# Performance work log

Measured on AMD Instinct MI355X. Metric: run time of the kernel, lower is better.

The kernel has to match this reference:

```python
import jax, jax.numpy as jnp
import numpy as np

B, T, DIM = 2, 2048, 1024
H, KVH, HD = 16, 4, 64
RANK = 32
QMAX = 31.0            # int6 signed: (1 << 5) - 1
SIGMA = 12.85          # MATRIX_QUANT_CLIP_SIGMAS
ROPE_BASE = 10000.0
LORA_SCALE = 1.0


def fake_quant_int6_rowwise(w):
    """Per-row int6 RTN fake-quant with clip-candidate search + STE, as in
    _quantize_rowwise_rtn / fake_quantize_int8_per_row (bits=6, no hessian)."""
    t = w.astype(jnp.float32)
    row_std = jnp.maximum(jnp.std(t, axis=1), 1e-8)                 # unbiased=False
    row_absmax = jnp.maximum(jnp.max(jnp.abs(t), axis=1), 1.0 / QMAX)
    # candidates: clip1 = max(std*sigma, absmax/qmax); clip2 = absmax (== initial best)
    s1 = jnp.maximum(jnp.maximum(row_std * SIGMA, row_absmax / QMAX) / QMAX, 1.0 / QMAX)
    s2 = jnp.maximum(row_absmax / QMAX, 1.0 / QMAX)
    q1 = jnp.clip(jnp.round(t / s1[:, None]), -QMAX, QMAX)
    q2 = jnp.clip(jnp.round(t / s2[:, None]), -QMAX, QMAX)
    e1 = jnp.mean((q1 * s1[:, None] - t) ** 2, axis=1)
    e2 = jnp.mean((q2 * s2[:, None] - t) ** 2, axis=1)
    use1 = e1 < e2  # torch keeps earlier/initial candidate on ties
    q = jnp.where(use1[:, None], q1, q2)
    s = jnp.where(use1, s1, s2)
    s = s.astype(jnp.float16).astype(jnp.float32)  # INT8_PER_ROW_SCALE_DTYPE
    w_deq = q * s[:, None]
    return w + jax.lax.stop_gradient(w_deq - w)   # straight-through estimator


def rope_tables(seq_len, head_dim):
    inv_freq = 1.0 / ROPE_BASE ** (np.arange(0, head_dim, 2, dtype=np.float32) / head_dim)
    freqs = np.arange(seq_len, dtype=np.float32)[:, None] * inv_freq[None, :]  # [T, HD/2]
    return jnp.asarray(np.cos(freqs)), jnp.asarray(np.sin(freqs))


def apply_rope(x, cos, sin):
    # x: [B, h, T, HD]; cos/sin: [T, HD/2]; rope_dims=0 -> rotate full head dim
    half = x.shape[-1] // 2
    x1, x2 = x[..., :half], x[..., half:]
    c = cos[None, None, :, :]
    s = sin[None, None, :, :]
    return jnp.concatenate([x1 * c + x2 * s, -x1 * s + x2 * c], axis=-1)


def setup_inputs() -> dict:
    key = jax.random.key(0)
    ks = jax.random.split(key, 16)
    d = {
        'x': jax.random.normal(ks[0], (B, T, DIM), jnp.float32),
        'Wq': jax.random.normal(ks[1], (DIM, DIM), jnp.float32) * 0.02,
        'Wk': jax.random.normal(ks[2], (KVH * HD, DIM), jnp.float32) * 0.02,
        'Wv': jax.random.normal(ks[3], (KVH * HD, DIM), jnp.float32) * 0.02,
        'Wo': jax.random.normal(ks[4], (DIM, DIM), jnp.float32) * 0.02,
        'qA': jax.random.normal(ks[5], (DIM, RANK), jnp.float32) * 0.02,
        'qB': jax.random.normal(ks[6], (RANK, DIM), jnp.float32) * 0.01,
        'kA': jax.random.normal(ks[7], (DIM, RANK), jnp.float32) * 0.02,
        'kB': jax.random.normal(ks[8], (RANK, KVH * HD), jnp.float32) * 0.01,
        'vA': jax.random.normal(ks[9], (DIM, RANK), jnp.float32) * 0.02,
        'vB': jax.random.normal(ks[10], (RANK, KVH * HD), jnp.float32) * 0.01,
        'pA': jax.random.normal(ks[11], (DIM, RANK), jnp.float32) * 0.02,
        'pB': jax.random.normal(ks[12], (RANK, DIM), jnp.float32) * 0.01,
        'q_gain': jnp.ones((H,), jnp.float32),
        'head_gate': jnp.ones((H,), jnp.float32),
    }
    return d


def reference(x, Wq, Wk, Wv, Wo, qA, qB, kA, kB, vA, vB, pA, pB, q_gain, head_gate):
    b, t, d = x.shape
    # QKV projections: fake-quantized base weight + LoRA low-rank add
    q = x @ fake_quant_int6_rowwise(Wq).T + LORA_SCALE * ((x @ qA) @ qB)
    k = x @ fake_quant_int6_rowwise(Wk).T + LORA_SCALE * ((x @ kA) @ kB)
    v = x @ fake_quant_int6_rowwise(Wv).T + LORA_SCALE * ((x @ vA) @ vB)

    q = q.reshape(b, t, H, HD).transpose(0, 2, 1, 3)      # [B, H, T, HD]
    k = k.reshape(b, t, KVH, HD).transpose(0, 2, 1, 3)    # [B, KVH, T, HD]
    v = v.reshape(b, t, KVH, HD).transpose(0, 2, 1, 3)

    cos, sin = rope_tables(t, HD)
    q = apply_rope(q, cos, sin) * q_gain[None, :, None, None]
    k = apply_rope(k, cos, sin)

    # GQA: expand kv heads to match query heads
    rep = H // KVH
    k = jnp.repeat(k, rep, axis=1)
    v = jnp.repeat(v, rep, axis=1)

    scores = jnp.einsum('bhqd,bhkd->bhqk', q, k) / np.sqrt(HD).astype(np.float32)
    causal = jnp.tril(jnp.ones((t, t), bool))
    scores = jnp.where(causal[None, None], scores, jnp.float32(-1e30))
    attn = jax.nn.softmax(scores, axis=-1)
    y = jnp.einsum('bhqk,bhkd->bhqd', attn, v)             # [B, H, T, HD]
    y = y * head_gate[None, :, None, None]
    y = y.transpose(0, 2, 1, 3).reshape(b, t, d)

    out = y @ fake_quant_int6_rowwise(Wo).T + LORA_SCALE * ((y @ pA) @ pB)
    return out
```

## Files before the change

### kernel.cpp

```cpp
#include <hip/hip_runtime.h>
#include <hip/hip_fp16.h>

#define Bc   2
#define Tc   2048
#define DIMc 1024
#define Hc   16
#define KVHc 4
#define HDc  64
#define Mc   4096

typedef unsigned short u16;
typedef __attribute__((ext_vector_type(8))) short short8;
typedef __attribute__((ext_vector_type(8))) __bf16 bf16x8;
typedef __attribute__((ext_vector_type(2))) __bf16 bf16x2;
typedef __attribute__((ext_vector_type(4))) float f32x4;
typedef __attribute__((ext_vector_type(4))) unsigned short u16x4;

typedef const __attribute__((address_space(1))) void* gas_t;
typedef __attribute__((address_space(3))) void* las_t;

#define L2E 1.4426950408889634f
#define L2B 0.41524101186092035f

__device__ inline float bf2f(u16 u) {
    unsigned int x = ((unsigned int)u) << 16;
    return __builtin_bit_cast(float, x);
}
__device__ inline u16 f2bf(float f) {
    unsigned int x = __builtin_bit_cast(unsigned int, f);
    x += 0x7fffu + ((x >> 16) & 1u);
    return (u16)(x >> 16);
}
__device__ inline unsigned int pkbf(float a, float b) {
#if __has_builtin(__builtin_amdgcn_cvt_pk_bf16_f32)
    bf16x2 r = __builtin_amdgcn_cvt_pk_bf16_f32(a, b);
    return __builtin_bit_cast(unsigned int, r);
#else
    return (unsigned int)f2bf(a) | ((unsigned int)f2bf(b) << 16);
#endif
}
__device__ inline u16x4 pk4(float a, float b, float c, float d) {
    uint2 u; u.x = pkbf(a, b); u.y = pkbf(c, d);
    return __builtin_bit_cast(u16x4, u);
}
__device__ inline float fexp2(float x) {
#if __has_builtin(__builtin_amdgcn_exp2f)
    return __builtin_amdgcn_exp2f(x);
#else
    return exp2f(x);
#endif
}
__device__ inline bf16x8 ld8(const u16* p) {
    return __builtin_bit_cast(bf16x8, *(const short8*)p);
}
__device__ inline f32x4 mfma16(bf16x8 a, bf16x8 b, f32x4 c) {
    return __builtin_amdgcn_mfma_f32_16x16x32_bf16(a, b, c, 0, 0, 0);
}
__device__ inline void gl_lds16(const u16* g, u16* l) {
    __builtin_amdgcn_global_load_lds((gas_t)g, (las_t)l, 16, 0, 0);
}

__global__ __launch_bounds__(256) void prep_kernel(
    const float* __restrict__ x,
    const float* __restrict__ qA, const float* __restrict__ kA,
    const float* __restrict__ vA, const float* __restrict__ pA,
    const float* __restrict__ qB, const float* __restrict__ kB,
    const float* __restrict__ vB, const float* __restrict__ pB,
    u16* __restrict__ x_bf, float* __restrict__ L)
{
    __shared__ __align__(16) u16 Ns[64 * 40];
    __shared__ __align__(16) u16 Ks[64 * 40];
    const int bx = blockIdx.x;
    const int tid = threadIdx.x;

    if (bx < 4096) {
        const int i = bx * 256 + tid;
        float4 v = ((const float4*)x)[i];
        ((u16x4*)x_bf)[i] = pk4(v.x, v.y, v.z, v.w);
        return;
    }
    const int lb = bx - 4096;
    const int mt = lb >> 4, kt = lb & 15;
    const int m0 = mt * 64, k0 = kt * 64;
    const float* Apt; const float* Bpt; int bdim, nnb;
    if (m0 < 1024)      { Apt = qA; Bpt = qB; bdim = 1024; nnb = m0; }
    else if (m0 < 1280) { Apt = kA; Bpt = kB; bdim = 256;  nnb = m0 - 1024; }
    else if (m0 < 1536) { Apt = vA; Bpt = vB; bdim = 256;  nnb = m0 - 1280; }
    else                { Apt = pA; Bpt = pB; bdim = 1024; nnb = m0 - 1536; }

    {
        const int row = tid >> 2, c0 = (tid & 3) * 8;
        const float4 f0 = *(const float4*)(Apt + (size_t)(k0 + row) * 32 + c0);
        const float4 f1 = *(const float4*)(Apt + (size_t)(k0 + row) * 32 + c0 + 4);
        *(u16x4*)&Ks[row * 40 + c0]     = pk4(f0.x, f0.y, f0.z, f0.w);
        *(u16x4*)&Ks[row * 40 + c0 + 4] = pk4(f1.x, f1.y, f1.z, f1.w);
    }
    {
        const int col = tid & 63;
        const int r0 = (tid >> 6) * 8;
        #pragma unroll
        for (int i = 0; i < 8; i++)
            Ns[col * 40 + r0 + i] = f2bf(Bpt[(size_t)(r0 + i) * bdim + nnb + col]);
    }
    __syncthreads();
    const int wave = tid >> 6, lane = tid & 63;
    const int quad = lane >> 4, l16 = lane & 15;
    const int wm = wave >> 1, wn = wave & 1;
    bf16x8 a0 = ld8(&Ns[(wm * 32 + l16) * 40 + quad * 8]);
    bf16x8 a1 = ld8(&Ns[(wm * 32 + 16 + l16) * 40 + quad * 8]);
    bf16x8 b0 = ld8(&Ks[(wn * 32 + l16) * 40 + quad * 8]);
    bf16x8 b1 = ld8(&Ks[(wn * 32 + 16 + l16) * 40 + quad * 8]);
    f32x4 c00 = {}, c01 = {}, c10 = {}, c11 = {};
    c00 = mfma16(a0, b0, c00);
    c01 = mfma16(a0, b1, c01);
    c10 = mfma16(a1, b0, c10);
    c11 = mfma16(a1, b1, c11);
    #pragma unroll
    for (int r = 0; r < 4; r++) {
        const size_t row_a = (size_t)(m0 + wm * 32 + quad * 4 + r) * 1024;
        const size_t row_b = (size_t)(m0 + wm * 32 + 16 + quad * 4 + r) * 1024;
        L[row_a + k0 + wn * 32 + l16]      = c00[r];
        L[row_a + k0 + wn * 32 + 16 + l16] = c01[r];
        L[row_b + k0 + wn * 32 + l16]      = c10[r];
        L[row_b + k0 + wn * 32 + 16 + l16] = c11[r];
    }
}

__device__ inline float block_sum(float v, volatile float* red) {
    #pragma unroll
    for (int off = 32; off; off >>= 1) v += __shfl_xor(v, off);
    __syncthreads();
    if ((threadIdx.x & 63) == 0) red[threadIdx.x >> 6] = v;
    __syncthreads();
    return red[0] + red[1] + red[2] + red[3];
}
__device__ inline float block_max(float v, volatile float* red) {
    #pragma unroll
    for (int off = 32; off; off >>= 1) v = fmaxf(v, __shfl_xor(v, off));
    __syncthreads();
    if ((threadIdx.x & 63) == 0) red[threadIdx.x >> 6] = v;
    __syncthreads();
    return fmaxf(fmaxf(red[0], red[1]), fmaxf(red[2], red[3]));
}

__global__ __launch_bounds__(256) void quant_kernel(
    const float* __restrict__ Wq, const float* __restrict__ Wk,
    const float* __restrict__ Wv, const float* __restrict__ Wo,
    const float* __restrict__ L,
    u16* __restrict__ Wqkv_b, u16* __restrict__ Wo_b)
{
    __shared__ float red[4];
    const int rblk = blockIdx.x;
    const int tid = threadIdx.x;
    const float* src; u16* dst;
    if (rblk < 1024)      { src = Wq + (size_t)rblk * DIMc;          dst = Wqkv_b + (size_t)rblk * DIMc; }
    else if (rblk < 1280) { src = Wk + (size_t)(rblk - 1024) * DIMc; dst = Wqkv_b + (size_t)rblk * DIMc; }
    else if (rblk < 1536) { src = Wv + (size_t)(rblk - 1280) * DIMc; dst = Wqkv_b + (size_t)rblk * DIMc; }
    else                  { src = Wo + (size_t)(rblk - 1536) * DIMc; dst = Wo_b + (size_t)(rblk - 1536) * DIMc; }

    float4 fv = ((const float4*)src)[tid];
    float tv[4] = {fv.x, fv.y, fv.z, fv.w};
    float ps = tv[0] + tv[1] + tv[2] + tv[3];
    float pa = fmaxf(fmaxf(fabsf(tv[0]), fabsf(tv[1])),
                     fmaxf(fabsf(tv[2]), fabsf(tv[3])));
    const float sum  = block_sum(ps, red);
    const float amax = block_max(pa, red);
    const float mean = sum * (1.0f / 1024.0f);
    float psq = 0.f;
    #pragma unroll
    for (int j = 0; j < 4; j++) { float d = tv[j] - mean; psq += d * d; }
    const float var  = block_sum(psq, red) * (1.0f / 1024.0f);
    const float row_std    = fmaxf(sqrtf(var), 1e-8f);
    const float row_absmax = fmaxf(amax, 1.0f / 31.0f);
    const float s1 = fmaxf(fmaxf(row_std * 12.85f, row_absmax * (1.0f / 31.0f)) * (1.0f / 31.0f),
                           1.0f / 31.0f);
    const float s2 = fmaxf(row_absmax * (1.0f / 31.0f), 1.0f / 31.0f);
    float pe1 = 0.f, pe2 = 0.f;
    #pragma unroll
    for (int j = 0; j < 4; j++) {
        float q1 = fminf(fmaxf(rintf(tv[j] / s1), -31.f), 31.f);
        float q2 = fminf(fmaxf(rintf(tv[j] / s2), -31.f), 31.f);
        float d1 = q1 * s1 - tv[j], d2 = q2 * s2 - tv[j];
        pe1 += d1 * d1; pe2 += d2 * d2;
    }
    const float e1 = block_sum(pe1, red);
    const float e2 = block_sum(pe2, red);
    const float ss = (e1 < e2) ? s1 : s2;
    const float sh = __half2float(__float2half(ss));

    const float4 lv = ((const float4*)(L + (size_t)rblk * 1024))[tid];
    const float lr[4] = {lv.x, lv.y, lv.z, lv.w};
    u16x4 outv;
    #pragma unroll
    for (int j = 0; j < 4; j++) {
        float q = fminf(fmaxf(rintf(tv[j] / ss), -31.f), 31.f);
        outv[j] = f2bf(q * sh + lr[j]);
    }
    ((u16x4*)dst)[tid] = outv;
}

__global__ __launch_bounds__(256) void gemm_tn(
    const u16* __restrict__ A, const u16* __restrict__ Bm, int K,
    int mode, float* __restrict__ Cf, int ldc,
    const float* __restrict__ q_gain,
    u16* __restrict__ qatt, u16* __restrict__ katt, u16* __restrict__ vatt)
{
    __shared__ __align__(16) u16 As[2][2048];
    __shared__ __align__(16) u16 Bs[2][4096];
    const int tid = threadIdx.x;
    const int wave = tid >> 6, lane = tid & 63;
    const int quad = lane >> 4, l16 = lane & 15;
    const int wm = wave >> 1, wn = wave & 1;
    const int tileM = blockIdx.y * 64, tileN = blockIdx.x * 128;

    const u16* Abase = A + (size_t)tileM * K;
    const u16* Bbase = Bm + (size_t)tileN * K;

    auto stage_it = [&](int k0, int buf) {
        {
            const int g = tid;
            const int r = g >> 2;
            const int cg = (g & 3) ^ (r & 3) ^ ((r >> 2) & 3);
            gl_lds16(Abase + (size_t)r * K + k0 + cg * 8, &As[buf][(size_t)g * 8]);
        }
        #pragma unroll
        for (int i = 0; i < 2; i++) {
            const int g = i * 256 + tid;
            const int r = g >> 2;
            const int cg = (g & 3) ^ (r & 3) ^ ((r >> 2) & 3);
            gl_lds16(Bbase + (size_t)r * K + k0 + cg * 8, &Bs[buf][(size_t)g * 8]);
        }
    };

    const int niter = K / 32;
    const int slot = quad ^ (l16 & 3) ^ ((l16 >> 2) & 3);
    f32x4 acc[2][4] = {};

    stage_it(0, 0);
    for (int it = 0; it < niter; it++) {
        const int buf = it & 1;
        __syncthreads();
        if (it + 1 < niter) stage_it((it + 1) * 32, buf ^ 1);
        bf16x8 af[2], bfr[4];
        #pragma unroll
        for (int mi = 0; mi < 2; mi++)
            af[mi] = ld8(&As[buf][(wm * 32 + mi * 16 + l16) * 32 + slot * 8]);
        #pragma unroll
        for (int ni = 0; ni < 4; ni++)
            bfr[ni] = ld8(&Bs[buf][(wn * 64 + ni * 16 + l16) * 32 + slot * 8]);
        #pragma unroll
        for (int mi = 0; mi < 2; mi++)
        #pragma unroll
        for (int ni = 0; ni < 4; ni++)
            acc[mi][ni] = mfma16(af[mi], bfr[ni], acc[mi][ni]);
    }

    const int row0 = tileM + wm * 32;
    const int col0 = tileN + wn * 64;
    if (mode == 0) {
        #pragma unroll
        for (int mi = 0; mi < 2; mi++)
        #pragma unroll
        for (int ni = 0; ni < 4; ni++)
        #pragma unroll
        for (int r = 0; r < 4; r++)
            Cf[(size_t)(row0 + mi * 16 + quad * 4 + r) * ldc + col0 + ni * 16 + l16]
                = acc[mi][ni][r];
        return;
    }
    const int bb = row0 >> 11;
    const int trow = row0 & (Tc - 1);
    if (col0 < 1024) {
        const int hh = col0 >> 6;
        const float g = q_gain[hh] * (0.125f * L2E);
        u16* qh = qatt + (size_t)(bb * Hc + hh) * Tc * HDc;
        #pragma unroll
        for (int ni = 0; ni < 2; ni++) {
            const int p = ni * 16 + l16;
            const float infr = fexp2(-L2B * (float)p);
            #pragma unroll
            for (int mi = 0; mi < 2; mi++) {
                #pragma unroll
                for (int r = 0; r < 4; r++) {
                    const int t = trow + mi * 16 + quad * 4 + r;
                    float s, c; __sincosf((float)t * infr, &s, &c);
                    const float x1 = acc[mi][ni][r], x2 = acc[mi][ni + 2][r];
                    qh[(size_t)t * HDc + p]      = f2bf((x1 * c + x2 * s) * g);
                    qh[(size_t)t * HDc + p + 32] = f2bf((x2 * c - x1 * s) * g);
                }
            }
        }
    } else if (col0 < 1280) {
        const int kvh = (col0 - 1024) >> 6;
        u16* kh = katt + (size_t)(bb * KVHc + kvh) * Tc * HDc;
        #pragma unroll
        for (int ni = 0; ni < 2; ni++) {
            const int p = ni * 16 + l16;
            const float infr = fexp2(-L2B * (float)p);
            #pragma unroll
            for (int mi = 0; mi < 2; mi++) {
                #pragma unroll
                for (int r = 0; r < 4; r++) {
                    const int t = trow + mi * 16 + quad * 4 + r;
                    float s, c; __sincosf((float)t * infr, &s, &c);
                    const float x1 = acc[mi][ni][r], x2 = acc[mi][ni + 2][r];
                    kh[(size_t)t * HDc + p]      = f2bf(x1 * c + x2 * s);
                    kh[(size_t)t * HDc + p + 32] = f2bf(x2 * c - x1 * s);
                }
            }
        }
    } else {
        const int kvh = (col0 - 1280) >> 6;
        u16* vh = vatt + (size_t)(bb * KVHc + kvh) * HDc * Tc;
        #pragma unroll
        for (int ni = 0; ni < 4; ni++) {
            const int hd = ni * 16 + l16;
            #pragma unroll
            for (int mi = 0; mi < 2; mi++) {
                const int t0 = trow + mi * 16 + quad * 4;
                u16x4 ov = pk4(acc[mi][ni][0], acc[mi][ni][1],
                               acc[mi][ni][2], acc[mi][ni][3]);
                *(u16x4*)(vh + (size_t)hd * Tc + t0) = ov;
            }
        }
    }
}

__global__ __launch_bounds__(256) void flash_attn6(
    const u16* __restrict__ qatt, const u16* __restrict__ katt,
    const u16* __restrict__ vatt, const float* __restrict__ head_gate,
    u16* __restrict__ ybf)
{
    __shared__ __align__(16) u16 sm[20480];
    const int tid = threadIdx.x;
    const int wv = tid >> 6, lane = tid & 63;
    const int quad = lane >> 4, l16 = lane & 15;
    const int sw = l16 & 7;
    const int bh = blockIdx.y;
    const int b = bh >> 4, h = bh & 15;
    const int kvh = h >> 2;
    const int x = blockIdx.x, s = bh >> 3;
    int qtile;
    if      (s == 0) qtile = x;
    else if (s == 1) qtile = 31 - x;
    else if (s == 2) qtile = (x + 8) & 31;
    else             qtile = 31 - ((x + 8) & 31);
    const int qw = qtile * 64 + wv * 16;
    const int nkt = qtile + 1;

    const u16* qbase = qatt + ((size_t)((b * Hc + h) * Tc + qw + l16)) * HDc;
    const bf16x8 bq0 = ld8(qbase + quad * 8);
    const bf16x8 bq1 = ld8(qbase + 32 + quad * 8);

    const u16* kbase = katt + (size_t)(b * KVHc + kvh) * Tc * HDc;
    const u16* vbase = vatt + (size_t)(b * KVHc + kvh) * HDc * Tc;

    auto stage = [&](int k0, int bb2) {
        #pragma unroll
        for (int i = 0; i < 2; i++) {
            const int g = wv * 128 + i * 64 + lane;
            const int r = g >> 3;
            const int cg = (g & 7) ^ (r & 7);
            gl_lds16(kbase + (size_t)(k0 + r) * HDc + cg * 8,
                     &sm[bb2 * 4096 + wv * 1024 + i * 512]);
            gl_lds16(vbase + (size_t)r * Tc + k0 + cg * 8,
                     &sm[8192 + bb2 * 4096 + wv * 1024 + i * 512]);
        }
    };

    float lsum = 0.f;
    f32x4 o[4] = {};
    u16* pw = &sm[16384 + wv * 1024];

    stage(0, 0);
    for (int kt = 0; kt < nkt; kt++) {
        const int bb2 = kt & 1;
        __syncthreads();
        if (kt + 1 < nkt) stage((kt + 1) * 64, bb2 ^ 1);

        const u16* Kb = &sm[bb2 * 4096];
        const u16* Vb = &sm[8192 + bb2 * 4096];
        f32x4 st[4];
        #pragma unroll
        for (int ft = 0; ft < 4; ft++) {
            const u16* kp = Kb + (ft * 16 + l16) * 64;
            bf16x8 a0 = ld8(kp + ((quad ^ sw) << 3));
            bf16x8 a1 = ld8(kp + (((quad + 4) ^ sw) << 3));
            f32x4 sacc = {};
            sacc = mfma16(a0, bq0, sacc);
            sacc = mfma16(a1, bq1, sacc);
            st[ft] = sacc;
        }
        if (kt == nkt - 1) {
            const int qloc = wv * 16 + l16;
            #pragma unroll
            for (int ft = 0; ft < 4; ft++)
                #pragma unroll
                for (int r = 0; r < 4; r++)
                    if (ft * 16 + quad * 4 + r > qloc) st[ft][r] = -1e30f;
        }
        #pragma unroll
        for (int ft = 0; ft < 4; ft++) {
            const float p0 = fexp2(st[ft][0]);
            const float p1 = fexp2(st[ft][1]);
            const float p2 = fexp2(st[ft][2]);
            const float p3 = fexp2(st[ft][3]);
            lsum += (p0 + p1) + (p2 + p3);
            const int c = (ft << 1) + (quad >> 1);
            u16* pd = &pw[(l16 << 6) + ((c ^ sw) << 3) + ((quad & 1) << 2)];
            uint2 pkv; pkv.x = pkbf(p0, p1); pkv.y = pkbf(p2, p3);
            *(uint2*)pd = pkv;
        }
        const bf16x8 pa0 = ld8(&pw[(l16 << 6) + ((quad ^ sw) << 3)]);
        const bf16x8 pa1 = ld8(&pw[(l16 << 6) + (((quad + 4) ^ sw) << 3)]);
        #pragma unroll
        for (int f = 0; f < 4; f++) {
            const u16* vp = Vb + (f * 16 + l16) * 64;
            bf16x8 v0 = ld8(vp + ((quad ^ sw) << 3));
            bf16x8 v1 = ld8(vp + (((quad + 4) ^ sw) << 3));
            o[f] = mfma16(v0, pa0, o[f]);
            o[f] = mfma16(v1, pa1, o[f]);
        }
    }
    lsum += __shfl_xor(lsum, 16);
    lsum += __shfl_xor(lsum, 32);
    const float inv = head_gate[h] / lsum;
    u16* yb = ybf + ((size_t)(b * Tc + qw + l16)) * DIMc + h * HDc + quad * 4;
    #pragma unroll
    for (int f = 0; f < 4; f++) {
        u16x4 pk = pk4(o[f][0] * inv, o[f][1] * inv,
                       o[f][2] * inv, o[f][3] * inv);
        *(u16x4*)(yb + f * 16) = pk;
    }
}

extern "C" void kernel_launch(void* const* d_in, const int* in_sizes, int n_in,
                              void* d_out, int out_size, void* d_ws, size_t ws_size,
                              hipStream_t stream) {
    (void)in_sizes; (void)n_in; (void)out_size; (void)ws_size;
    const float* x    = (const float*)d_in[0];
    const float* Wq   = (const float*)d_in[1];
    const float* Wk   = (const float*)d_in[2];
    const float* Wv   = (const float*)d_in[3];
    const float* Wo   = (const float*)d_in[4];
    const float* qA   = (const float*)d_in[5];
    const float* qB   = (const float*)d_in[6];
    const float* kA   = (const float*)d_in[7];
    const float* kB   = (const float*)d_in[8];
    const float* vA   = (const float*)d_in[9];
    const float* vB   = (const float*)d_in[10];
    const float* pA   = (const float*)d_in[11];
    const float* pB   = (const float*)d_in[12];
    const float* q_gain    = (const float*)d_in[13];
    const float* head_gate = (const float*)d_in[14];
    float* out = (float*)d_out;

    char* wsp = (char*)d_ws;
    size_t off = 0;
    auto alloc = [&](size_t bytes) -> void* {
        void* p = wsp + off;
        off = (off + bytes + 255) & ~(size_t)255;
        return p;
    };
    u16* x_bf    = (u16*)alloc((size_t)Mc * DIMc * 2);
    float* Lbuf  = (float*)alloc((size_t)2560 * 1024 * 4);
    u16* Wqkv_b  = (u16*)alloc((size_t)1536 * DIMc * 2);
    u16* Wo_b    = (u16*)alloc((size_t)DIMc * DIMc * 2);
    u16* qatt    = (u16*)alloc((size_t)Mc * DIMc * 2);
    u16* katt    = (u16*)alloc((size_t)Mc * 256 * 2);
    u16* vatt    = (u16*)alloc((size_t)Mc * 256 * 2);
    u16* y_bf    = (u16*)alloc((size_t)Mc * DIMc * 2);

    prep_kernel<<<4736, 256, 0, stream>>>(x, qA, kA, vA, pA, qB, kB, vB, pB,
                                          x_bf, Lbuf);

    quant_kernel<<<2560, 256, 0, stream>>>(Wq, Wk, Wv, Wo, Lbuf, Wqkv_b, Wo_b);

    gemm_tn<<<dim3(12, 64), 256, 0, stream>>>(x_bf, Wqkv_b, DIMc,
                                              2, nullptr, 0,
                                              q_gain, qatt, katt, vatt);

    flash_attn6<<<dim3(32, Bc * Hc), 256, 0, stream>>>(qatt, katt, vatt, head_gate, y_bf);

    gemm_tn<<<dim3(8, 64), 256, 0, stream>>>(y_bf, Wo_b, DIMc,
                                             0, out, DIMc,
                                             nullptr, nullptr, nullptr, nullptr);
}
```

Measured before the change: 191.8 us.

## Process 128-query tiles per block with two 16-row query groups per wave

The attention kernel now handles 128 queries per block, with each wave owning 32 query rows as two 16-row groups. Each K/V tile staged in LDS is therefore reused by twice as many queries, and the grid shrinks from 32 to 16 tiles per head. Waves skip the diagonal tile they do not need, and the old four-way tile reordering is replaced by a simpler per-batch reversal. In exchange each thread holds more registers and the block uses more LDS, so occupancy may drop, and there are fewer blocks to spread load across the GPU.

```diff
diff --git a/kernel.cpp b/kernel.cpp
--- a/kernel.cpp
+++ b/kernel.cpp
@@ -326,12 +326,12 @@
     }
 }
 
-__global__ __launch_bounds__(256) void flash_attn6(
+__global__ __launch_bounds__(256) void flash_attn7(
     const u16* __restrict__ qatt, const u16* __restrict__ katt,
     const u16* __restrict__ vatt, const float* __restrict__ head_gate,
     u16* __restrict__ ybf)
 {
-    __shared__ __align__(16) u16 sm[20480];
+    __shared__ __align__(16) u16 sm[24576];
     const int tid = threadIdx.x;
     const int wv = tid >> 6, lane = tid & 63;
     const int quad = lane >> 4, l16 = lane & 15;
@@ -339,18 +339,16 @@
     const int bh = blockIdx.y;
     const int b = bh >> 4, h = bh & 15;
     const int kvh = h >> 2;
-    const int x = blockIdx.x, s = bh >> 3;
-    int qtile;
-    if      (s == 0) qtile = x;
-    else if (s == 1) qtile = 31 - x;
-    else if (s == 2) qtile = (x + 8) & 31;
-    else             qtile = 31 - ((x + 8) & 31);
-    const int qw = qtile * 64 + wv * 16;
-    const int nkt = qtile + 1;
+    const int qtile = b ? (15 - (int)blockIdx.x) : (int)blockIdx.x;
+    const int qw = qtile * 128 + wv * 32;
+    const int nkt = 2 * qtile + 2;
+    const int ktmax_w = 2 * qtile + (wv >> 1);
 
     const u16* qbase = qatt + ((size_t)((b * Hc + h) * Tc + qw + l16)) * HDc;
-    const bf16x8 bq0 = ld8(qbase + quad * 8);
-    const bf16x8 bq1 = ld8(qbase + 32 + quad * 8);
+    const bf16x8 bqa0 = ld8(qbase + quad * 8);
+    const bf16x8 bqa1 = ld8(qbase + 32 + quad * 8);
+    const bf16x8 bqb0 = ld8(qbase + 16 * HDc + quad * 8);
+    const bf16x8 bqb1 = ld8(qbase + 16 * HDc + 32 + quad * 8);
 
     const u16* kbase = katt + (size_t)(b * KVHc + kvh) * Tc * HDc;
     const u16* vbase = vatt + (size_t)(b * KVHc + kvh) * HDc * Tc;
@@ -368,69 +366,88 @@
         }
     };
 
-    float lsum = 0.f;
-    f32x4 o[4] = {};
-    u16* pw = &sm[16384 + wv * 1024];
+    float lsa = 0.f, lsb = 0.f;
+    f32x4 oa[4] = {}, ob[4] = {};
+    u16* pw = &sm[16384 + wv * 2048];
 
     stage(0, 0);
     for (int kt = 0; kt < nkt; kt++) {
         const int bb2 = kt & 1;
         __syncthreads();
         if (kt + 1 < nkt) stage((kt + 1) * 64, bb2 ^ 1);
+        if (kt > ktmax_w) continue;
 
         const u16* Kb = &sm[bb2 * 4096];
         const u16* Vb = &sm[8192 + bb2 * 4096];
-        f32x4 st[4];
+        f32x4 sta[4], stb[4];
         #pragma unroll
         for (int ft = 0; ft < 4; ft++) {
             const u16* kp = Kb + (ft * 16 + l16) * 64;
             bf16x8 a0 = ld8(kp + ((quad ^ sw) << 3));
             bf16x8 a1 = ld8(kp + (((quad + 4) ^ sw) << 3));
-            f32x4 sacc = {};
-            sacc = mfma16(a0, bq0, sacc);
-            sacc = mfma16(a1, bq1, sacc);
-            st[ft] = sacc;
-        }
-        if (kt == nkt - 1) {
-            const int qloc = wv * 16 + l16;
+            f32x4 s = {};
+            s = mfma16(a0, bqa0, s); s = mfma16(a1, bqa1, s);
+            sta[ft] = s;
+            f32x4 s2 = {};
+            s2 = mfma16(a0, bqb0, s2); s2 = mfma16(a1, bqb1, s2);
+            stb[ft] = s2;
+        }
+        if (kt == ktmax_w) {
+            const int kb0 = kt * 64;
+            const int qa = qw + l16, qb = qw + 16 + l16;
             #pragma unroll
             for (int ft = 0; ft < 4; ft++)
                 #pragma unroll
-                for (int r = 0; r < 4; r++)
-                    if (ft * 16 + quad * 4 + r > qloc) st[ft][r] = -1e30f;
+                for (int r = 0; r < 4; r++) {
+                    const int key = kb0 + ft * 16 + quad * 4 + r;
+                    if (key > qa) sta[ft][r] = -1e30f;
+                    if (key > qb) stb[ft][r] = -1e30f;
+                }
         }
         #pragma unroll
         for (int ft = 0; ft < 4; ft++) {
-            const float p0 = fexp2(st[ft][0]);
-            const float p1 = fexp2(st[ft][1]);
-            const float p2 = fexp2(st[ft][2]);
-            const float p3 = fexp2(st[ft][3]);
-            lsum += (p0 + p1) + (p2 + p3);
             const int c = (ft << 1) + (quad >> 1);
-            u16* pd = &pw[(l16 << 6) + ((c ^ sw) << 3) + ((quad & 1) << 2)];
+            const int co = ((c ^ sw) << 3) + ((quad & 1) << 2);
+            float p0 = fexp2(sta[ft][0]), p1 = fexp2(sta[ft][1]);
+            float p2 = fexp2(sta[ft][2]), p3 = fexp2(sta[ft][3]);
+            lsa += (p0 + p1) + (p2 + p3);
             uint2 pkv; pkv.x = pkbf(p0, p1); pkv.y = pkbf(p2, p3);
-            *(uint2*)pd = pkv;
-        }
-        const bf16x8 pa0 = ld8(&pw[(l16 << 6) + ((quad ^ sw) << 3)]);
-        const bf16x8 pa1 = ld8(&pw[(l16 << 6) + (((quad + 4) ^ sw) << 3)]);
+            *(uint2*)&pw[(l16 << 6) + co] = pkv;
+            p0 = fexp2(stb[ft][0]); p1 = fexp2(stb[ft][1]);
+            p2 = fexp2(stb[ft][2]); p3 = fexp2(stb[ft][3]);
+            lsb += (p0 + p1) + (p2 + p3);
+            pkv.x = pkbf(p0, p1); pkv.y = pkbf(p2, p3);
+            *(uint2*)&pw[((16 + l16) << 6) + co] = pkv;
+        }
+        const bf16x8 paa0 = ld8(&pw[(l16 << 6) + ((quad ^ sw) << 3)]);
+        const bf16x8 paa1 = ld8(&pw[(l16 << 6) + (((quad + 4) ^ sw) << 3)]);
+        const bf16x8 pab0 = ld8(&pw[((16 + l16) << 6) + ((quad ^ sw) << 3)]);
+        const bf16x8 pab1 = ld8(&pw[((16 + l16) << 6) + (((quad + 4) ^ sw) << 3)]);
         #pragma unroll
         for (int f = 0; f < 4; f++) {
             const u16* vp = Vb + (f * 16 + l16) * 64;
             bf16x8 v0 = ld8(vp + ((quad ^ sw) << 3));
             bf16x8 v1 = ld8(vp + (((quad + 4) ^ sw) << 3));
-            o[f] = mfma16(v0, pa0, o[f]);
-            o[f] = mfma16(v1, pa1, o[f]);
-        }
-    }
-    lsum += __shfl_xor(lsum, 16);
-    lsum += __shfl_xor(lsum, 32);
-    const float inv = head_gate[h] / lsum;
-    u16* yb = ybf + ((size_t)(b * Tc + qw + l16)) * DIMc + h * HDc + quad * 4;
+            oa[f] = mfma16(v0, paa0, oa[f]);
+            oa[f] = mfma16(v1, paa1, oa[f]);
+            ob[f] = mfma16(v0, pab0, ob[f]);
+            ob[f] = mfma16(v1, pab1, ob[f]);
+        }
+    }
+    lsa += __shfl_xor(lsa, 16); lsa += __shfl_xor(lsa, 32);
+    lsb += __shfl_xor(lsb, 16); lsb += __shfl_xor(lsb, 32);
+    const float g = head_gate[h];
+    const float inva = g / lsa, invb = g / lsb;
+    u16* yba = ybf + ((size_t)(b * Tc + qw + l16)) * DIMc + h * HDc + quad * 4;
+    u16* ybb = ybf + ((size_t)(b * Tc + qw + 16 + l16)) * DIMc + h * HDc + quad * 4;
     #pragma unroll
     for (int f = 0; f < 4; f++) {
-        u16x4 pk = pk4(o[f][0] * inv, o[f][1] * inv,
-                       o[f][2] * inv, o[f][3] * inv);
-        *(u16x4*)(yb + f * 16) = pk;
+        u16x4 pka = pk4(oa[f][0] * inva, oa[f][1] * inva,
+                        oa[f][2] * inva, oa[f][3] * inva);
+        *(u16x4*)(yba + f * 16) = pka;
+        u16x4 pkb = pk4(ob[f][0] * invb, ob[f][1] * invb,
+                        ob[f][2] * invb, ob[f][3] * invb);
+        *(u16x4*)(ybb + f * 16) = pkb;
     }
 }
 
@@ -480,7 +497,7 @@
                                               2, nullptr, 0,
                                               q_gain, qatt, katt, vatt);
 
-    flash_attn6<<<dim3(32, Bc * Hc), 256, 0, stream>>>(qatt, katt, vatt, head_gate, y_bf);
+    flash_attn7<<<dim3(16, Bc * Hc), 256, 0, stream>>>(qatt, katt, vatt, head_gate, y_bf);
 
     gemm_tn<<<dim3(8, 64), 256, 0, stream>>>(y_bf, Wo_b, DIMc,
                                              0, out, DIMc,
```

Result: slower. 197.0 us (+2.7%).
